# Kernel optimization log

Measured on AMD Instinct MI355X. Metric: run time of the kernel, lower is better.

## Reference

```python
import jax, jax.numpy as jnp
import numpy as np
from jax.scipy.special import logsumexp

# config (matches init_kwargs)
D_IN, D_OUT = 768, 256
P = 2
BLUR = 0.5
SCALING = 0.8
SCALING_FACTOR = 1.0
N_ITERS = 36  # fixed-length eps schedule (clamped at blur), jit-friendly


def setup_inputs() -> dict:
    key = jax.random.key(0)
    k1, k2, k3, k4 = jax.random.split(key, 4)
    d = jax.random.normal(k1, (4096, D_IN), dtype=jnp.float32)
    s1 = jax.random.normal(k2, (1024, D_IN), dtype=jnp.float32)
    s2 = jax.random.normal(k3, (1024, D_IN), dtype=jnp.float32)
    # learned projection parameter (scaled init so projected coords are O(1))
    M = jax.random.normal(k4, (D_IN, D_OUT), dtype=jnp.float32) / np.sqrt(D_IN)
    return {"d": d, "s1": s1, "s2": s2, "M": M}


def _sq_cost(u, v):
    # C[i,j] = ||u_i - v_j||^2 / 2  (geomloss p=2 cost)
    sq = (jnp.sum(u * u, -1)[:, None] + jnp.sum(v * v, -1)[None, :]
          - 2.0 * (u @ v.T))
    return jnp.maximum(sq, 0.0) * 0.5


def _softmin(eps, C, h):
    # -eps * log sum_j exp(h_j - C_ij/eps)   -> shape [C.shape[0]]
    return -eps * logsumexp(h[None, :] - C / eps, axis=1)


def _sinkhorn_divergence(x, y):
    n, m = x.shape[0], y.shape[0]
    a_log = jnp.full((n,), -np.log(n), dtype=x.dtype)  # uniform log-weights
    b_log = jnp.full((m,), -np.log(m), dtype=x.dtype)

    C_xy = _sq_cost(x, y)   # [n, m]
    C_xx = _sq_cost(x, x)   # [n, n]  (debiasing term)
    C_yy = _sq_cost(y, y)   # [m, m]

    # bounding-box diameter of the joint cloud (no grad, like geomloss)
    z = jax.lax.stop_gradient(jnp.concatenate([x, y], axis=0))
    diam = jnp.sqrt(jnp.sum((z.max(0) - z.min(0)) ** 2)) + 1e-6

    # eps-scaling schedule: scale from diameter down to blur, eps = scale^p
    scales = jnp.maximum(BLUR, diam * (SCALING ** jnp.arange(N_ITERS, dtype=x.dtype)))
    eps_list = scales ** P
    eps0 = eps_list[0]
    eps_f = jnp.asarray(BLUR ** P, dtype=x.dtype)

    # init potentials at the largest eps
    f_aa = _softmin(eps0, C_xx, a_log)
    g_bb = _softmin(eps0, C_yy, b_log)
    f_ab = _softmin(eps0, C_xy, b_log)
    g_ab = _softmin(eps0, C_xy.T, a_log)

    @jax.checkpoint
    def step(carry, eps):
        f_aa, g_bb, f_ab, g_ab = carry
        # simultaneous (Jacobi) updates, symmetrized by averaging
        ft = _softmin(eps, C_xy, b_log + g_ab / eps)
        gt = _softmin(eps, C_xy.T, a_log + f_ab / eps)
        f_aa = 0.5 * (f_aa + _softmin(eps, C_xx, a_log + f_aa / eps))
        g_bb = 0.5 * (g_bb + _softmin(eps, C_yy, b_log + g_bb / eps))
        f_ab = 0.5 * (f_ab + ft)
        g_ab = 0.5 * (g_ab + gt)
        return (f_aa, g_bb, f_ab, g_ab), None

    (f_aa, g_bb, f_ab, g_ab), _ = jax.lax.scan(
        step, (f_aa, g_bb, f_ab, g_ab), eps_list)

    # final non-averaged extrapolation at eps = blur^p
    f_ab_n = _softmin(eps_f, C_xy, b_log + g_ab / eps_f)
    g_ab_n = _softmin(eps_f, C_xy.T, a_log + f_ab / eps_f)
    f_aa_n = _softmin(eps_f, C_xx, a_log + f_aa / eps_f)
    g_bb_n = _softmin(eps_f, C_yy, b_log + g_bb / eps_f)

    # debiased divergence with uniform weights: <a, f_ab - f_aa> + <b, g_ab - g_bb>
    return jnp.mean(f_ab_n - f_aa_n) + jnp.mean(g_ab_n - g_bb_n)


def reference(d, s1, s2, M):
    xd = d @ M
    x1 = s1 @ M
    x2 = s2 @ M
    dist1 = _sinkhorn_divergence(xd, x1)
    dist2 = _sinkhorn_divergence(xd, x2)
    return jax.nn.sigmoid(SCALING_FACTOR * (dist2 - dist1))
```

## Files before the change

kernel.cpp:

```cpp
#include <hip/hip_runtime.h>
#include <hip/hip_bf16.h>
#include <math.h>

using ull = unsigned long long;
typedef unsigned short u16x8 __attribute__((ext_vector_type(8)));
typedef __attribute__((ext_vector_type(8))) short bf16x8;
typedef __attribute__((ext_vector_type(4))) float f32x4;

#define ND 4096ull
#define NS 1024ull
#define DOUT 256ull
#define DIN 768ull
#define NIT 36

constexpr ull U_CXX = 0;
constexpr ull U_CXY = U_CXX + ND*ND;
constexpr ull U_CYX = U_CXY + 2*ND*NS;
constexpr ull U_CYY = U_CYX + 2*ND*NS;
constexpr ull U_TOT = U_CYY + 2*NS*NS;
constexpr ull P_XDH = U_TOT;
constexpr ull P_XDM = P_XDH + ND*DOUT;
constexpr ull P_X1H = P_XDM + ND*DOUT;
constexpr ull P_X1M = P_X1H + NS*DOUT;
constexpr ull P_X2H = P_X1M + NS*DOUT;
constexpr ull P_X2M = P_X2H + NS*DOUT;
constexpr ull P_DH  = P_X2M + NS*DOUT;
constexpr ull P_DM  = P_DH + ND*DIN;
constexpr ull P_S1H = P_DM + ND*DIN;
constexpr ull P_S1M = P_S1H + NS*DIN;
constexpr ull P_S2H = P_S1M + NS*DIN;
constexpr ull P_S2M = P_S2H + NS*DIN;
constexpr ull P_MTH = P_S2M + NS*DIN;
constexpr ull P_MTM = P_MTH + DOUT*DIN;
constexpr ull U_END = P_MTM + DOUT*DIN;

constexpr ull O_XD   = U_END / 2;
constexpr ull O_X1   = O_XD + ND*DOUT;
constexpr ull O_X2   = O_X1 + NS*DOUT;
constexpr ull O_MT   = O_X2 + NS*DOUT;
constexpr ull O_ND_  = O_MT + DOUT*DIN;
constexpr ull O_N1   = O_ND_ + ND;
constexpr ull O_N2   = O_N1 + NS;
constexpr ull O_FAB  = O_N2 + NS;
constexpr ull O_GAB  = O_FAB + 4*ND;
constexpr ull O_FAA  = O_GAB + 4*NS;
constexpr ull O_GBB  = O_FAA + 4*ND;
constexpr ull O_FABN = O_GBB + 4*NS;
constexpr ull O_GABN = O_FABN + 2*ND;
constexpr ull O_FAAN = O_GABN + 2*NS;
constexpr ull O_GBBN = O_FAAN + 2*ND;
constexpr ull O_EPS  = O_GBBN + 2*NS;
constexpr ull O_QS   = O_EPS + 2*NIT;
constexpr ull O_DIST = O_QS + 2;
constexpr ull WS_FLOATS = O_DIST + 2;
constexpr ull O_PMIN = O_MT;
constexpr ull O_PMAX = O_MT + 96*256;

constexpr float LOG2E = 1.4426950408889634f;
constexpr float LN2   = 0.69314718055994531f;
constexpr float A_LOG2 = -12.0f;
constexpr float B_LOG2 = -10.0f;

__device__ __forceinline__ float wave_max(float v) {
    #pragma unroll
    for (int o = 32; o; o >>= 1) v = fmaxf(v, __shfl_xor(v, o));
    return v;
}
__device__ __forceinline__ float wave_sum(float v) {
    #pragma unroll
    for (int o = 32; o; o >>= 1) v += __shfl_xor(v, o);
    return v;
}

__device__ __forceinline__ unsigned short f2bf_rn(float x) {
    union { float f; unsigned u; } v; v.f = x;
    const unsigned r = v.u + 0x7FFFu + ((v.u >> 16) & 1u);
    return (unsigned short)(r >> 16);
}
__device__ __forceinline__ float bf2f(unsigned short b) {
    union { unsigned u; float f; } v; v.u = ((unsigned)b) << 16; return v.f;
}

__global__ __launch_bounds__(256)
void transpose_M_k(const float* __restrict__ M, float* __restrict__ Mt)
{
    int idx = blockIdx.x * 256 + threadIdx.x;
    int r = idx >> 8;
    int c = idx & 255;
    Mt[(size_t)c * DIN + r] = M[idx];
}

__global__ __launch_bounds__(256)
void pack_bf16_gen(const float* __restrict__ X,
                   unsigned short* __restrict__ Phi, unsigned short* __restrict__ Pmi,
                   int KB)
{
    const int p = blockIdx.x;
    const int t = threadIdx.x;
    const int K = KB * 32;
    for (int s = t; s < KB * 64; s += 256) {
        const int kb = s >> 6, l = s & 63;
        const int row = p * 16 + (l & 15);
        const int k0 = kb * 32 + ((l >> 4) << 3);
        const float* src = X + (ull)row * K + k0;
        u16x8 hi, mi;
        #pragma unroll
        for (int e = 0; e < 8; e++) {
            const float x = src[e];
            const unsigned short h = f2bf_rn(x);
            hi[e] = h;
            mi[e] = f2bf_rn(x - bf2f(h));
        }
        const ull o = (((ull)p * KB + kb) * 64 + l) * 8;
        *(u16x8*)&Phi[o] = hi;
        *(u16x8*)&Pmi[o] = mi;
    }
}

__global__ __launch_bounds__(256)
void gemm_proj_mfma(const unsigned short* __restrict__ Ahi, const unsigned short* __restrict__ Ami,
                    const unsigned short* __restrict__ Bhi, const unsigned short* __restrict__ Bmi,
                    float* __restrict__ C, int N, int KB)
{
    const int l = threadIdx.x & 63;
    const int w = threadIdx.x >> 6;
    const int n0 = blockIdx.x * 64, m0 = blockIdx.y * 128;
    const int pA0 = (m0 >> 4) + w * 2;
    const int pB0 = n0 >> 4;
    f32x4 acc[2][4] = {};
    for (int kb = 0; kb < KB; kb++) {
        const ull a0o = (((ull)(pA0 + 0) * KB + kb) * 64 + l) * 8;
        const ull a1o = (((ull)(pA0 + 1) * KB + kb) * 64 + l) * 8;
        const bf16x8 aH0 = *(const bf16x8*)&Ahi[a0o];
        const bf16x8 aM0 = *(const bf16x8*)&Ami[a0o];
        const bf16x8 aH1 = *(const bf16x8*)&Ahi[a1o];
        const bf16x8 aM1 = *(const bf16x8*)&Ami[a1o];
        #pragma unroll
        for (int j = 0; j < 4; j++) {
            const ull bo = (((ull)(pB0 + j) * KB + kb) * 64 + l) * 8;
            const bf16x8 bH = *(const bf16x8*)&Bhi[bo];
            const bf16x8 bM = *(const bf16x8*)&Bmi[bo];
            acc[0][j] = __builtin_amdgcn_mfma_f32_16x16x32_bf16(aH0, bH, acc[0][j], 0, 0, 0);
            acc[0][j] = __builtin_amdgcn_mfma_f32_16x16x32_bf16(aH0, bM, acc[0][j], 0, 0, 0);
            acc[0][j] = __builtin_amdgcn_mfma_f32_16x16x32_bf16(aM0, bH, acc[0][j], 0, 0, 0);
            acc[1][j] = __builtin_amdgcn_mfma_f32_16x16x32_bf16(aH1, bH, acc[1][j], 0, 0, 0);
            acc[1][j] = __builtin_amdgcn_mfma_f32_16x16x32_bf16(aH1, bM, acc[1][j], 0, 0, 0);
            acc[1][j] = __builtin_amdgcn_mfma_f32_16x16x32_bf16(aM1, bH, acc[1][j], 0, 0, 0);
        }
    }
    const int col = l & 15;
    #pragma unroll
    for (int i = 0; i < 2; i++) {
        const int row0 = m0 + w * 32 + i * 16 + ((l >> 4) << 2);
        #pragma unroll
        for (int r = 0; r < 4; r++) {
            const ull rowb = (ull)(row0 + r) * N + n0;
            #pragma unroll
            for (int j = 0; j < 4; j++)
                C[rowb + j * 16 + col] = acc[i][j][r];
        }
    }
}

__device__ __forceinline__ unsigned int quant16(float c, float s) {
    return __float2uint_rn(fminf(c * s, 65535.0f));
}

__global__ __launch_bounds__(256)
void gemm_cost_mfma(const unsigned short* __restrict__ Ahi, const unsigned short* __restrict__ Ami,
                    const unsigned short* __restrict__ Bhi, const unsigned short* __restrict__ Bmi,
                    unsigned short* __restrict__ C,
                    const float* __restrict__ na, const float* __restrict__ nb,
                    const float* __restrict__ qsp, int N)
{
    const int l = threadIdx.x & 63;
    const int w = threadIdx.x >> 6;
    const int n0 = blockIdx.x * 64, m0 = blockIdx.y * 128;
    const int pA0 = (m0 >> 4) + w * 2;
    const int pB0 = n0 >> 4;
    f32x4 acc[2][4] = {};
    #pragma unroll
    for (int kb = 0; kb < 8; kb++) {
        const ull a0o = (((ull)(pA0 + 0) * 8 + kb) * 64 + l) * 8;
        const ull a1o = (((ull)(pA0 + 1) * 8 + kb) * 64 + l) * 8;
        const bf16x8 aH0 = *(const bf16x8*)&Ahi[a0o];
        const bf16x8 aM0 = *(const bf16x8*)&Ami[a0o];
        const bf16x8 aH1 = *(const bf16x8*)&Ahi[a1o];
        const bf16x8 aM1 = *(const bf16x8*)&Ami[a1o];
        #pragma unroll
        for (int j = 0; j < 4; j++) {
            const ull bo = (((ull)(pB0 + j) * 8 + kb) * 64 + l) * 8;
            const bf16x8 bH = *(const bf16x8*)&Bhi[bo];
            const bf16x8 bM = *(const bf16x8*)&Bmi[bo];
            acc[0][j] = __builtin_amdgcn_mfma_f32_16x16x32_bf16(aH0, bH, acc[0][j], 0, 0, 0);
            acc[0][j] = __builtin_amdgcn_mfma_f32_16x16x32_bf16(aH0, bM, acc[0][j], 0, 0, 0);
            acc[0][j] = __builtin_amdgcn_mfma_f32_16x16x32_bf16(aM0, bH, acc[0][j], 0, 0, 0);
            acc[1][j] = __builtin_amdgcn_mfma_f32_16x16x32_bf16(aH1, bH, acc[1][j], 0, 0, 0);
            acc[1][j] = __builtin_amdgcn_mfma_f32_16x16x32_bf16(aH1, bM, acc[1][j], 0, 0, 0);
            acc[1][j] = __builtin_amdgcn_mfma_f32_16x16x32_bf16(aM1, bH, acc[1][j], 0, 0, 0);
        }
    }
    const float s = qsp[0];
    const int col = l & 15;
    float nbj[4];
    #pragma unroll
    for (int j = 0; j < 4; j++) nbj[j] = nb[n0 + j * 16 + col];
    #pragma unroll
    for (int i = 0; i < 2; i++) {
        const int row0 = m0 + w * 32 + i * 16 + ((l >> 4) << 2);
        #pragma unroll
        for (int r = 0; r < 4; r++) {
            const float nar = na[row0 + r];
            const ull rowb = (ull)(row0 + r) * N + n0;
            #pragma unroll
            for (int j = 0; j < 4; j++)
                C[rowb + j * 16 + col] =
                    (unsigned short)quant16(0.5f * fmaxf(nar + nbj[j] - 2.0f * acc[i][j][r], 0.0f), s);
        }
    }
}

__global__ __launch_bounds__(256)
void row_norm(const float* __restrict__ x, float* __restrict__ o)
{
    const int i = blockIdx.x;
    const float v = x[(size_t)i * DOUT + threadIdx.x];
    float s = wave_sum(v * v);
    __shared__ float red[4];
    const int wid = threadIdx.x >> 6, lane = threadIdx.x & 63;
    if (lane == 0) red[wid] = s;
    __syncthreads();
    if (threadIdx.x == 0) o[i] = red[0] + red[1] + red[2] + red[3];
}

__global__ __launch_bounds__(256)
void colminmax_k(const float* __restrict__ xd, const float* __restrict__ x1,
                 const float* __restrict__ x2, float* __restrict__ ws)
{
    const int b = blockIdx.x, c = threadIdx.x;
    const float* src; int r0;
    if (b < 64)      { src = xd; r0 = b * 64; }
    else if (b < 80) { src = x1; r0 = (b - 64) * 64; }
    else             { src = x2; r0 = (b - 80) * 64; }
    float mn = 3.4e38f, mx = -3.4e38f;
    for (int r = 0; r < 64; r++) {
        const float v = src[(size_t)(r0 + r) * DOUT + c];
        mn = fminf(mn, v); mx = fmaxf(mx, v);
    }
    ws[O_PMIN + (ull)b * 256 + c] = mn;
    ws[O_PMAX + (ull)b * 256 + c] = mx;
}

__global__ __launch_bounds__(256)
void eps_k(float* __restrict__ ws)
{
    const int c = threadIdx.x;
    const float* pmin = ws + O_PMIN;
    const float* pmax = ws + O_PMAX;
    float mnd = 3.4e38f, mxd = -3.4e38f;
    float mn1 = 3.4e38f, mx1 = -3.4e38f;
    float mn2 = 3.4e38f, mx2 = -3.4e38f;
    for (int b = 0;  b < 64; b++) { mnd = fminf(mnd, pmin[b*256+c]); mxd = fmaxf(mxd, pmax[b*256+c]); }
    for (int b = 64; b < 80; b++) { mn1 = fminf(mn1, pmin[b*256+c]); mx1 = fmaxf(mx1, pmax[b*256+c]); }
    for (int b = 80; b < 96; b++) { mn2 = fminf(mn2, pmin[b*256+c]); mx2 = fmaxf(mx2, pmax[b*256+c]); }
    const float d1 = fmaxf(mxd, mx1) - fminf(mnd, mn1);
    const float d2 = fmaxf(mxd, mx2) - fminf(mnd, mn2);
    float s1 = wave_sum(d1 * d1);
    float s2 = wave_sum(d2 * d2);
    __shared__ float r1[4], r2[4];
    const int wid = c >> 6, lane = c & 63;
    if (lane == 0) { r1[wid] = s1; r2[wid] = s2; }
    __syncthreads();
    if (c == 0) {
        const float d1s = r1[0]+r1[1]+r1[2]+r1[3];
        const float d2s = r2[0]+r2[1]+r2[2]+r2[3];
        const float cb = 0.5f * fmaxf(d1s, d2s) * 1.02f + 1.0f;
        ws[O_QS]     = 65535.0f / cb;
        ws[O_QS + 1] = cb / 65535.0f;
    }
    if (c < 2 * NIT) {
        const int div = c / NIT, tt = c % NIT;
        const float ss = div ? (r2[0]+r2[1]+r2[2]+r2[3]) : (r1[0]+r1[1]+r1[2]+r1[3]);
        const float diam = sqrtf(ss) + 1e-6f;
        const float sc = fmaxf(0.5f, diam * powf(0.8f, (float)tt));
        ws[O_EPS + (ull)div * NIT + tt] = sc * sc;
    }
}

__device__ __forceinline__ void softmin_1k(
    const unsigned short* __restrict__ Cseg, const float* __restrict__ hseg,
    float hc2, float ie2, float qsc, int lane, float& mO, float& sO)
{
    float v[16];
    #pragma unroll
    for (int c = 0; c < 2; c++) {
        const int off = c * 512 + lane * 8;
        const u16x8 q = *(const u16x8*)&Cseg[off];
        if (hseg) {
            const float4 ha = *(const float4*)&hseg[off];
            const float4 hb = *(const float4*)&hseg[off + 4];
            const float hv[8] = {ha.x, ha.y, ha.z, ha.w, hb.x, hb.y, hb.z, hb.w};
            #pragma unroll
            for (int e = 0; e < 8; e++)
                v[c*8 + e] = fmaf((float)q[e], qsc, fmaf(hv[e], ie2, hc2));
        } else {
            #pragma unroll
            for (int e = 0; e < 8; e++)
                v[c*8 + e] = fmaf((float)q[e], qsc, hc2);
        }
    }
    float m = v[0];
    #pragma unroll
    for (int k = 1; k < 16; k++) m = fmaxf(m, v[k]);
    m = wave_max(m);
    float s = 0.0f;
    #pragma unroll
    for (int k = 0; k < 16; k++) s += exp2f(v[k] - m);
    sO = wave_sum(s);
    mO = m;
}

__global__ __launch_bounds__(256)
void sinkhorn_phase(float* __restrict__ ws, int phase, int t)
{
    __shared__ float mS[8], sS[8];
    const unsigned short* uq = (const unsigned short*)ws;
    const int wid = threadIdx.x >> 6, lane = threadIdx.x & 63;
    const float qs = ws[O_QS + 1];
    int rb, wb;
    if (phase == 0) { rb = 0; wb = 0; }
    else { rb = t & 1; wb = rb ^ 1; }
    const int b = blockIdx.x;

    if (b < 2048) {
        const int div = b >> 10;
        const int i = ((b & 1023) << 2) + wid;
        const float eps = (phase == 2) ? 0.25f : ws[O_EPS + (ull)div * NIT + t];
        const float ie2 = LOG2E / eps, qsc = -qs * ie2;
        const unsigned short* Crow = uq + U_CXY + (ull)div * ND * NS + (ull)i * NS;
        const float* h    = phase ? (ws + O_GAB + ((ull)div * 2 + rb) * NS) : nullptr;
        const float* self = ws + O_FAB + ((ull)div * 2 + rb) * ND;
        float* outp = (phase == 2) ? (ws + O_FABN + (ull)div * ND)
                                   : (ws + O_FAB + ((ull)div * 2 + wb) * ND);
        float m, s;
        softmin_1k(Crow, h, B_LOG2, ie2, qsc, lane, m, s);
        if (lane == 0) {
            float res = -eps * LN2 * (m + log2f(s));
            if (phase == 1) res = 0.5f * (self[i] + res);
            outp[i] = res;
        }
    } else if (b < 4096) {
        const int q = b - 2048, div = q >> 10, j = q & 1023;
        const float eps = (phase == 2) ? 0.25f : ws[O_EPS + (ull)div * NIT + t];
        const float ie2 = LOG2E / eps, qsc = -qs * ie2;
        const unsigned short* Cseg = uq + U_CYX + (ull)div * ND * NS + (ull)j * ND + wid * 1024;
        const float* h    = phase ? (ws + O_FAB + ((ull)div * 2 + rb) * ND + wid * 1024) : nullptr;
        const float* self = ws + O_GAB + ((ull)div * 2 + rb) * NS;
        float* outp = (phase == 2) ? (ws + O_GABN + (ull)div * NS)
                                   : (ws + O_GAB + ((ull)div * 2 + wb) * NS);
        float m, s;
        softmin_1k(Cseg, h, A_LOG2, ie2, qsc, lane, m, s);
        if (lane == 0) { mS[wid] = m; sS[wid] = s; }
        __syncthreads();
        if (threadIdx.x == 0) {
            const float m0 = fmaxf(fmaxf(mS[0], mS[1]), fmaxf(mS[2], mS[3]));
            const float st = sS[0]*exp2f(mS[0]-m0) + sS[1]*exp2f(mS[1]-m0)
                           + sS[2]*exp2f(mS[2]-m0) + sS[3]*exp2f(mS[3]-m0);
            float res = -eps * LN2 * (m0 + log2f(st));
            if (phase == 1) res = 0.5f * (self[j] + res);
            outp[j] = res;
        }
    } else if (b < 8192) {
        const int i = b - 4096;
        const float eps0 = (phase == 2) ? 0.25f : ws[O_EPS + t];
        const float eps1 = (phase == 2) ? 0.25f : ws[O_EPS + NIT + t];
        const float ie0 = LOG2E / eps0, qs0 = -qs * ie0;
        const float ie1 = LOG2E / eps1, qs1 = -qs * ie1;
        const unsigned short* Cseg = uq + U_CXX + (ull)i * ND + wid * 1024;
        const float* h0b = ws + O_FAA + (ull)rb * ND;
        const float* h1b = ws + O_FAA + (2ull + rb) * ND;
        float* out0 = (phase == 2) ? (ws + O_FAAN)      : (ws + O_FAA + (ull)wb * ND);
        float* out1 = (phase == 2) ? (ws + O_FAAN + ND) : (ws + O_FAA + (2ull + wb) * ND);
        float v0[16], v1[16];
        #pragma unroll
        for (int c = 0; c < 2; c++) {
            const int off = c * 512 + lane * 8;
            const u16x8 q = *(const u16x8*)&Cseg[off];
            float cq[8];
            #pragma unroll
            for (int e = 0; e < 8; e++) cq[e] = (float)q[e];
            if (phase) {
                const int go = wid * 1024 + off;
                const float4 a0 = *(const float4*)&h0b[go];
                const float4 b0 = *(const float4*)&h0b[go + 4];
                const float4 a1 = *(const float4*)&h1b[go];
                const float4 b1 = *(const float4*)&h1b[go + 4];
                const float h0v[8] = {a0.x, a0.y, a0.z, a0.w, b0.x, b0.y, b0.z, b0.w};
                const float h1v[8] = {a1.x, a1.y, a1.z, a1.w, b1.x, b1.y, b1.z, b1.w};
                #pragma unroll
                for (int e = 0; e < 8; e++) {
                    v0[c*8 + e] = fmaf(cq[e], qs0, fmaf(h0v[e], ie0, A_LOG2));
                    v1[c*8 + e] = fmaf(cq[e], qs1, fmaf(h1v[e], ie1, A_LOG2));
                }
            } else {
                #pragma unroll
                for (int e = 0; e < 8; e++) {
                    v0[c*8 + e] = fmaf(cq[e], qs0, A_LOG2);
                    v1[c*8 + e] = fmaf(cq[e], qs1, A_LOG2);
                }
            }
        }
        float m0 = v0[0], m1 = v1[0];
        #pragma unroll
        for (int k = 1; k < 16; k++) { m0 = fmaxf(m0, v0[k]); m1 = fmaxf(m1, v1[k]); }
        m0 = wave_max(m0); m1 = wave_max(m1);
        float s0 = 0.0f, s1 = 0.0f;
        #pragma unroll
        for (int k = 0; k < 16; k++) { s0 += exp2f(v0[k] - m0); s1 += exp2f(v1[k] - m1); }
        s0 = wave_sum(s0); s1 = wave_sum(s1);
        if (lane == 0) { mS[wid] = m0; sS[wid] = s0; mS[4 + wid] = m1; sS[4 + wid] = s1; }
        __syncthreads();
        if (threadIdx.x == 0) {
            const float ma = fmaxf(fmaxf(mS[0], mS[1]), fmaxf(mS[2], mS[3]));
            const float sa = sS[0]*exp2f(mS[0]-ma) + sS[1]*exp2f(mS[1]-ma)
                           + sS[2]*exp2f(mS[2]-ma) + sS[3]*exp2f(mS[3]-ma);
            float r0 = -eps0 * LN2 * (ma + log2f(sa));
            if (phase == 1) r0 = 0.5f * (h0b[i] + r0);
            out0[i] = r0;
            const float mb = fmaxf(fmaxf(mS[4], mS[5]), fmaxf(mS[6], mS[7]));
            const float sb = sS[4]*exp2f(mS[4]-mb) + sS[5]*exp2f(mS[5]-mb)
                           + sS[6]*exp2f(mS[6]-mb) + sS[7]*exp2f(mS[7]-mb);
            float r1 = -eps1 * LN2 * (mb + log2f(sb));
            if (phase == 1) r1 = 0.5f * (h1b[i] + r1);
            out1[i] = r1;
        }
    } else {
        const int q = b - 8192, div = q >> 8;
        const int i = ((q & 255) << 2) + wid;
        const float eps = (phase == 2) ? 0.25f : ws[O_EPS + (ull)div * NIT + t];
        const float ie2 = LOG2E / eps, qsc = -qs * ie2;
        const unsigned short* Crow = uq + U_CYY + (ull)div * NS * NS + (ull)i * NS;
        const float* hb = ws + O_GBB + ((ull)div * 2 + rb) * NS;
        float* outp = (phase == 2) ? (ws + O_GBBN + (ull)div * NS)
                                   : (ws + O_GBB + ((ull)div * 2 + wb) * NS);
        float m, s;
        softmin_1k(Crow, phase ? hb : nullptr, B_LOG2, ie2, qsc, lane, m, s);
        if (lane == 0) {
            float res = -eps * LN2 * (m + log2f(s));
            if (phase == 1) res = 0.5f * (hb[i] + res);
            outp[i] = res;
        }
    }
}

__global__ __launch_bounds__(256)
void reduce_dist(float* __restrict__ ws)
{
    const int d = blockIdx.x;
    const int tix = threadIdx.x;
    float s = 0.0f;
    #pragma unroll
    for (int k = 0; k < 16; k++) {
        const int i = tix + k * 256;
        s += (ws[O_FABN + (ull)d * ND + i] - ws[O_FAAN + (ull)d * ND + i]) * (1.0f / 4096.0f);
    }
    #pragma unroll
    for (int k = 0; k < 4; k++) {
        const int j = tix + k * 256;
        s += (ws[O_GABN + (ull)d * NS + j] - ws[O_GBBN + (ull)d * NS + j]) * (1.0f / 1024.0f);
    }
    s = wave_sum(s);
    __shared__ float red[4];
    const int wid = tix >> 6, lane = tix & 63;
    if (lane == 0) red[wid] = s;
    __syncthreads();
    if (tix == 0) ws[O_DIST + d] = red[0] + red[1] + red[2] + red[3];
}

__global__ void finalize_k(const float* __restrict__ ws, float* __restrict__ out)
{
    const float x = ws[O_DIST + 1] - ws[O_DIST + 0];
    out[0] = 1.0f / (1.0f + expf(-x));
}

extern "C" void kernel_launch(void* const* d_in, const int* in_sizes, int n_in,
                              void* d_out, int out_size, void* d_ws, size_t ws_size,
                              hipStream_t stream)
{
    if (ws_size < WS_FLOATS * sizeof(float)) return;

    const float* dmat = (const float*)d_in[0];
    const float* s1   = (const float*)d_in[1];
    const float* s2   = (const float*)d_in[2];
    const float* M    = (const float*)d_in[3];
    float* ws  = (float*)d_ws;
    float* out = (float*)d_out;
    unsigned short* uq = (unsigned short*)d_ws;

    float* Mt = ws + O_MT;
    float* xd = ws + O_XD;
    float* x1 = ws + O_X1;
    float* x2 = ws + O_X2;

    transpose_M_k<<<768, 256, 0, stream>>>(M, Mt);
    pack_bf16_gen<<<256, 256, 0, stream>>>(dmat, uq + P_DH,  uq + P_DM,  24);
    pack_bf16_gen<<<64,  256, 0, stream>>>(s1,   uq + P_S1H, uq + P_S1M, 24);
    pack_bf16_gen<<<64,  256, 0, stream>>>(s2,   uq + P_S2H, uq + P_S2M, 24);
    pack_bf16_gen<<<16,  256, 0, stream>>>(Mt,   uq + P_MTH, uq + P_MTM, 24);
    gemm_proj_mfma<<<dim3(4, 32), 256, 0, stream>>>(uq+P_DH,  uq+P_DM,  uq+P_MTH, uq+P_MTM, xd, 256, 24);
    gemm_proj_mfma<<<dim3(4, 8),  256, 0, stream>>>(uq+P_S1H, uq+P_S1M, uq+P_MTH, uq+P_MTM, x1, 256, 24);
    gemm_proj_mfma<<<dim3(4, 8),  256, 0, stream>>>(uq+P_S2H, uq+P_S2M, uq+P_MTH, uq+P_MTM, x2, 256, 24);
    row_norm<<<4096, 256, 0, stream>>>(xd, ws + O_ND_);
    row_norm<<<1024, 256, 0, stream>>>(x1, ws + O_N1);
    row_norm<<<1024, 256, 0, stream>>>(x2, ws + O_N2);
    colminmax_k<<<96, 256, 0, stream>>>(xd, x1, x2, ws);
    eps_k<<<1, 256, 0, stream>>>(ws);
    pack_bf16_gen<<<256, 256, 0, stream>>>(xd, uq + P_XDH, uq + P_XDM, 8);
    pack_bf16_gen<<<64,  256, 0, stream>>>(x1, uq + P_X1H, uq + P_X1M, 8);
    pack_bf16_gen<<<64,  256, 0, stream>>>(x2, uq + P_X2H, uq + P_X2M, 8);
    const float* qsp = ws + O_QS;
    const float* nd_ = ws + O_ND_;
    const float* n1  = ws + O_N1;
    const float* n2  = ws + O_N2;
    gemm_cost_mfma<<<dim3(64, 32), 256, 0, stream>>>(uq+P_XDH, uq+P_XDM, uq+P_XDH, uq+P_XDM, uq + U_CXX,         nd_, nd_, qsp, 4096);
    gemm_cost_mfma<<<dim3(16, 32), 256, 0, stream>>>(uq+P_XDH, uq+P_XDM, uq+P_X1H, uq+P_X1M, uq + U_CXY,         nd_, n1,  qsp, 1024);
    gemm_cost_mfma<<<dim3(64, 8),  256, 0, stream>>>(uq+P_X1H, uq+P_X1M, uq+P_XDH, uq+P_XDM, uq + U_CYX,         n1,  nd_, qsp, 4096);
    gemm_cost_mfma<<<dim3(16, 32), 256, 0, stream>>>(uq+P_XDH, uq+P_XDM, uq+P_X2H, uq+P_X2M, uq + U_CXY + ND*NS, nd_, n2,  qsp, 1024);
    gemm_cost_mfma<<<dim3(64, 8),  256, 0, stream>>>(uq+P_X2H, uq+P_X2M, uq+P_XDH, uq+P_XDM, uq + U_CYX + ND*NS, n2,  nd_, qsp, 4096);
    gemm_cost_mfma<<<dim3(16, 8),  256, 0, stream>>>(uq+P_X1H, uq+P_X1M, uq+P_X1H, uq+P_X1M, uq + U_CYY,         n1,  n1,  qsp, 1024);
    gemm_cost_mfma<<<dim3(16, 8),  256, 0, stream>>>(uq+P_X2H, uq+P_X2M, uq+P_X2H, uq+P_X2M, uq + U_CYY + NS*NS, n2,  n2,  qsp, 1024);
    sinkhorn_phase<<<8704, 256, 0, stream>>>(ws, 0, 0);
    for (int t = 0; t < NIT; t++)
        sinkhorn_phase<<<8704, 256, 0, stream>>>(ws, 1, t);
    sinkhorn_phase<<<8704, 256, 0, stream>>>(ws, 2, 36);
    reduce_dist<<<2, 256, 0, stream>>>(ws);
    finalize_k<<<1, 1, 0, stream>>>(ws, out);
}
```

Before: 1.194 ms.

## Split softmin rows across twice as many waves with 512-thread blocks

Blocks in the Sinkhorn phase kernel go from 256 to 512 threads. Each wave now handles a 512-element segment instead of 1024, and partial max/sum pairs are merged through shared memory (pairs for the row-wise cases, eight-way for the column and self-cost cases). This doubles the wave count per iteration and halves per-thread work and register use, aiming for more memory-level parallelism on the streaming softmin. In exchange it adds block-wide syncs and extra shared-memory combine work in every block.

Result: slower. 1.376 ms (+15.2%).

```diff
diff --git a/kernel.cpp b/kernel.cpp
--- a/kernel.cpp
+++ b/kernel.cpp
@@ -287,43 +287,39 @@
     }
 }
 
-__device__ __forceinline__ void softmin_1k(
+__device__ __forceinline__ void softmin_512(
     const unsigned short* __restrict__ Cseg, const float* __restrict__ hseg,
     float hc2, float ie2, float qsc, int lane, float& mO, float& sO)
 {
-    float v[16];
-    #pragma unroll
-    for (int c = 0; c < 2; c++) {
-        const int off = c * 512 + lane * 8;
-        const u16x8 q = *(const u16x8*)&Cseg[off];
-        if (hseg) {
-            const float4 ha = *(const float4*)&hseg[off];
-            const float4 hb = *(const float4*)&hseg[off + 4];
-            const float hv[8] = {ha.x, ha.y, ha.z, ha.w, hb.x, hb.y, hb.z, hb.w};
-            #pragma unroll
-            for (int e = 0; e < 8; e++)
-                v[c*8 + e] = fmaf((float)q[e], qsc, fmaf(hv[e], ie2, hc2));
-        } else {
-            #pragma unroll
-            for (int e = 0; e < 8; e++)
-                v[c*8 + e] = fmaf((float)q[e], qsc, hc2);
-        }
+    float v[8];
+    const u16x8 q = *(const u16x8*)&Cseg[lane * 8];
+    if (hseg) {
+        const float4 ha = *(const float4*)&hseg[lane * 8];
+        const float4 hb = *(const float4*)&hseg[lane * 8 + 4];
+        const float hv[8] = {ha.x, ha.y, ha.z, ha.w, hb.x, hb.y, hb.z, hb.w};
+        #pragma unroll
+        for (int e = 0; e < 8; e++)
+            v[e] = fmaf((float)q[e], qsc, fmaf(hv[e], ie2, hc2));
+    } else {
+        #pragma unroll
+        for (int e = 0; e < 8; e++)
+            v[e] = fmaf((float)q[e], qsc, hc2);
     }
     float m = v[0];
     #pragma unroll
-    for (int k = 1; k < 16; k++) m = fmaxf(m, v[k]);
+    for (int k = 1; k < 8; k++) m = fmaxf(m, v[k]);
     m = wave_max(m);
     float s = 0.0f;
     #pragma unroll
-    for (int k = 0; k < 16; k++) s += exp2f(v[k] - m);
+    for (int k = 0; k < 8; k++) s += exp2f(v[k] - m);
     sO = wave_sum(s);
     mO = m;
 }
 
-__global__ __launch_bounds__(256)
+__global__ __launch_bounds__(512)
 void sinkhorn_phase(float* __restrict__ ws, int phase, int t)
 {
-    __shared__ float mS[8], sS[8];
+    __shared__ float mS[16], sS[16];
     const unsigned short* uq = (const unsigned short*)ws;
     const int wid = threadIdx.x >> 6, lane = threadIdx.x & 63;
     const float qs = ws[O_QS + 1];
@@ -333,19 +329,23 @@
     const int b = blockIdx.x;
 
     if (b < 2048) {
-        const int div = b >> 10;
-        const int i = ((b & 1023) << 2) + wid;
+        const int g = (b << 2) + (wid >> 1);
+        const int div = g >> 12, i = g & 4095, seg = wid & 1;
         const float eps = (phase == 2) ? 0.25f : ws[O_EPS + (ull)div * NIT + t];
         const float ie2 = LOG2E / eps, qsc = -qs * ie2;
-        const unsigned short* Crow = uq + U_CXY + (ull)div * ND * NS + (ull)i * NS;
-        const float* h    = phase ? (ws + O_GAB + ((ull)div * 2 + rb) * NS) : nullptr;
+        const unsigned short* Cseg = uq + U_CXY + (ull)div * ND * NS + (ull)i * NS + seg * 512;
+        const float* h    = phase ? (ws + O_GAB + ((ull)div * 2 + rb) * NS + seg * 512) : nullptr;
         const float* self = ws + O_FAB + ((ull)div * 2 + rb) * ND;
         float* outp = (phase == 2) ? (ws + O_FABN + (ull)div * ND)
                                    : (ws + O_FAB + ((ull)div * 2 + wb) * ND);
         float m, s;
-        softmin_1k(Crow, h, B_LOG2, ie2, qsc, lane, m, s);
-        if (lane == 0) {
-            float res = -eps * LN2 * (m + log2f(s));
+        softmin_512(Cseg, h, B_LOG2, ie2, qsc, lane, m, s);
+        if (lane == 0) { mS[wid] = m; sS[wid] = s; }
+        __syncthreads();
+        if (seg == 0 && lane == 0) {
+            const float m0 = fmaxf(mS[wid], mS[wid + 1]);
+            const float st = sS[wid]*exp2f(mS[wid]-m0) + sS[wid+1]*exp2f(mS[wid+1]-m0);
+            float res = -eps * LN2 * (m0 + log2f(st));
             if (phase == 1) res = 0.5f * (self[i] + res);
             outp[i] = res;
         }
@@ -353,19 +353,22 @@
         const int q = b - 2048, div = q >> 10, j = q & 1023;
         const float eps = (phase == 2) ? 0.25f : ws[O_EPS + (ull)div * NIT + t];
         const float ie2 = LOG2E / eps, qsc = -qs * ie2;
-        const unsigned short* Cseg = uq + U_CYX + (ull)div * ND * NS + (ull)j * ND + wid * 1024;
-        const float* h    = phase ? (ws + O_FAB + ((ull)div * 2 + rb) * ND + wid * 1024) : nullptr;
+        const unsigned short* Cseg = uq + U_CYX + (ull)div * ND * NS + (ull)j * ND + wid * 512;
+        const float* h    = phase ? (ws + O_FAB + ((ull)div * 2 + rb) * ND + wid * 512) : nullptr;
         const float* self = ws + O_GAB + ((ull)div * 2 + rb) * NS;
         float* outp = (phase == 2) ? (ws + O_GABN + (ull)div * NS)
                                    : (ws + O_GAB + ((ull)div * 2 + wb) * NS);
         float m, s;
-        softmin_1k(Cseg, h, A_LOG2, ie2, qsc, lane, m, s);
+        softmin_512(Cseg, h, A_LOG2, ie2, qsc, lane, m, s);
         if (lane == 0) { mS[wid] = m; sS[wid] = s; }
         __syncthreads();
         if (threadIdx.x == 0) {
-            const float m0 = fmaxf(fmaxf(mS[0], mS[1]), fmaxf(mS[2], mS[3]));
-            const float st = sS[0]*exp2f(mS[0]-m0) + sS[1]*exp2f(mS[1]-m0)
-                           + sS[2]*exp2f(mS[2]-m0) + sS[3]*exp2f(mS[3]-m0);
+            float m0 = mS[0];
+            #pragma unroll
+            for (int k = 1; k < 8; k++) m0 = fmaxf(m0, mS[k]);
+            float st = 0.0f;
+            #pragma unroll
+            for (int k = 0; k < 8; k++) st += sS[k] * exp2f(mS[k] - m0);
             float res = -eps * LN2 * (m0 + log2f(st));
             if (phase == 1) res = 0.5f * (self[j] + res);
             outp[j] = res;
@@ -376,21 +379,19 @@
         const float eps1 = (phase == 2) ? 0.25f : ws[O_EPS + NIT + t];
         const float ie0 = LOG2E / eps0, qs0 = -qs * ie0;
         const float ie1 = LOG2E / eps1, qs1 = -qs * ie1;
-        const unsigned short* Cseg = uq + U_CXX + (ull)i * ND + wid * 1024;
+        const unsigned short* Cseg = uq + U_CXX + (ull)i * ND + wid * 512;
         const float* h0b = ws + O_FAA + (ull)rb * ND;
         const float* h1b = ws + O_FAA + (2ull + rb) * ND;
         float* out0 = (phase == 2) ? (ws + O_FAAN)      : (ws + O_FAA + (ull)wb * ND);
         float* out1 = (phase == 2) ? (ws + O_FAAN + ND) : (ws + O_FAA + (2ull + wb) * ND);
-        float v0[16], v1[16];
-        #pragma unroll
-        for (int c = 0; c < 2; c++) {
-            const int off = c * 512 + lane * 8;
-            const u16x8 q = *(const u16x8*)&Cseg[off];
+        float v0[8], v1[8];
+        {
+            const u16x8 q = *(const u16x8*)&Cseg[lane * 8];
             float cq[8];
             #pragma unroll
             for (int e = 0; e < 8; e++) cq[e] = (float)q[e];
             if (phase) {
-                const int go = wid * 1024 + off;
+                const int go = wid * 512 + lane * 8;
                 const float4 a0 = *(const float4*)&h0b[go];
                 const float4 b0 = *(const float4*)&h0b[go + 4];
                 const float4 a1 = *(const float4*)&h1b[go];
@@ -399,54 +400,66 @@
                 const float h1v[8] = {a1.x, a1.y, a1.z, a1.w, b1.x, b1.y, b1.z, b1.w};
                 #pragma unroll
                 for (int e = 0; e < 8; e++) {
-                    v0[c*8 + e] = fmaf(cq[e], qs0, fmaf(h0v[e], ie0, A_LOG2));
-                    v1[c*8 + e] = fmaf(cq[e], qs1, fmaf(h1v[e], ie1, A_LOG2));
+                    v0[e] = fmaf(cq[e], qs0, fmaf(h0v[e], ie0, A_LOG2));
+                    v1[e] = fmaf(cq[e], qs1, fmaf(h1v[e], ie1, A_LOG2));
                 }
             } else {
                 #pragma unroll
                 for (int e = 0; e < 8; e++) {
-                    v0[c*8 + e] = fmaf(cq[e], qs0, A_LOG2);
-                    v1[c*8 + e] = fmaf(cq[e], qs1, A_LOG2);
+                    v0[e] = fmaf(cq[e], qs0, A_LOG2);
+                    v1[e] = fmaf(cq[e], qs1, A_LOG2);
                 }
             }
         }
         float m0 = v0[0], m1 = v1[0];
         #pragma unroll
-        for (int k = 1; k < 16; k++) { m0 = fmaxf(m0, v0[k]); m1 = fmaxf(m1, v1[k]); }
+        for (int k = 1; k < 8; k++) { m0 = fmaxf(m0, v0[k]); m1 = fmaxf(m1, v1[k]); }
         m0 = wave_max(m0); m1 = wave_max(m1);
         float s0 = 0.0f, s1 = 0.0f;
         #pragma unroll
-        for (int k = 0; k < 16; k++) { s0 += exp2f(v0[k] - m0); s1 += exp2f(v1[k] - m1); }
+        for (int k = 0; k < 8; k++) { s0 += exp2f(v0[k] - m0); s1 += exp2f(v1[k] - m1); }
         s0 = wave_sum(s0); s1 = wave_sum(s1);
-        if (lane == 0) { mS[wid] = m0; sS[wid] = s0; mS[4 + wid] = m1; sS[4 + wid] = s1; }
+        if (lane == 0) { mS[wid] = m0; sS[wid] = s0; mS[8 + wid] = m1; sS[8 + wid] = s1; }
         __syncthreads();
         if (threadIdx.x == 0) {
-            const float ma = fmaxf(fmaxf(mS[0], mS[1]), fmaxf(mS[2], mS[3]));
-            const float sa = sS[0]*exp2f(mS[0]-ma) + sS[1]*exp2f(mS[1]-ma)
-                           + sS[2]*exp2f(mS[2]-ma) + sS[3]*exp2f(mS[3]-ma);
+            float ma = mS[0];
+            #pragma unroll
+            for (int k = 1; k < 8; k++) ma = fmaxf(ma, mS[k]);
+            float sa = 0.0f;
+            #pragma unroll
+            for (int k = 0; k < 8; k++) sa += sS[k] * exp2f(mS[k] - ma);
             float r0 = -eps0 * LN2 * (ma + log2f(sa));
             if (phase == 1) r0 = 0.5f * (h0b[i] + r0);
             out0[i] = r0;
-            const float mb = fmaxf(fmaxf(mS[4], mS[5]), fmaxf(mS[6], mS[7]));
-            const float sb = sS[4]*exp2f(mS[4]-mb) + sS[5]*exp2f(mS[5]-mb)
-                           + sS[6]*exp2f(mS[6]-mb) + sS[7]*exp2f(mS[7]-mb);
+            float mb = mS[8];
+            #pragma unroll
+            for (int k = 9; k < 16; k++) mb = fmaxf(mb, mS[k]);
+            float sb = 0.0f;
+            #pragma unroll
+            for (int k = 8; k < 16; k++) sb += sS[k] * exp2f(mS[k] - mb);
             float r1 = -eps1 * LN2 * (mb + log2f(sb));
             if (phase == 1) r1 = 0.5f * (h1b[i] + r1);
             out1[i] = r1;
         }
     } else {
-        const int q = b - 8192, div = q >> 8;
-        const int i = ((q & 255) << 2) + wid;
+        const int q = b - 8192;
+        const int g = (q << 2) + (wid >> 1);
+        const int div = g >> 10, i = g & 1023, seg = wid & 1;
         const float eps = (phase == 2) ? 0.25f : ws[O_EPS + (ull)div * NIT + t];
         const float ie2 = LOG2E / eps, qsc = -qs * ie2;
-        const unsigned short* Crow = uq + U_CYY + (ull)div * NS * NS + (ull)i * NS;
+        const unsigned short* Cseg = uq + U_CYY + (ull)div * NS * NS + (ull)i * NS + seg * 512;
         const float* hb = ws + O_GBB + ((ull)div * 2 + rb) * NS;
+        const float* h = phase ? (hb + seg * 512) : nullptr;
         float* outp = (phase == 2) ? (ws + O_GBBN + (ull)div * NS)
                                    : (ws + O_GBB + ((ull)div * 2 + wb) * NS);
         float m, s;
-        softmin_1k(Crow, phase ? hb : nullptr, B_LOG2, ie2, qsc, lane, m, s);
-        if (lane == 0) {
-            float res = -eps * LN2 * (m + log2f(s));
+        softmin_512(Cseg, h, B_LOG2, ie2, qsc, lane, m, s);
+        if (lane == 0) { mS[wid] = m; sS[wid] = s; }
+        __syncthreads();
+        if (seg == 0 && lane == 0) {
+            const float m0 = fmaxf(mS[wid], mS[wid + 1]);
+            const float st = sS[wid]*exp2f(mS[wid]-m0) + sS[wid+1]*exp2f(mS[wid+1]-m0);
+            float res = -eps * LN2 * (m0 + log2f(st));
             if (phase == 1) res = 0.5f * (hb[i] + res);
             outp[i] = res;
         }
@@ -529,10 +542,10 @@
     gemm_cost_mfma<<<dim3(64, 8),  256, 0, stream>>>(uq+P_X2H, uq+P_X2M, uq+P_XDH, uq+P_XDM, uq + U_CYX + ND*NS, n2,  nd_, qsp, 4096);
     gemm_cost_mfma<<<dim3(16, 8),  256, 0, stream>>>(uq+P_X1H, uq+P_X1M, uq+P_X1H, uq+P_X1M, uq + U_CYY,         n1,  n1,  qsp, 1024);
     gemm_cost_mfma<<<dim3(16, 8),  256, 0, stream>>>(uq+P_X2H, uq+P_X2M, uq+P_X2H, uq+P_X2M, uq + U_CYY + NS*NS, n2,  n2,  qsp, 1024);
-    sinkhorn_phase<<<8704, 256, 0, stream>>>(ws, 0, 0);
+    sinkhorn_phase<<<8704, 512, 0, stream>>>(ws, 0, 0);
     for (int t = 0; t < NIT; t++)
-        sinkhorn_phase<<<8704, 256, 0, stream>>>(ws, 1, t);
-    sinkhorn_phase<<<8704, 256, 0, stream>>>(ws, 2, 36);
+        sinkhorn_phase<<<8704, 512, 0, stream>>>(ws, 1, t);
+    sinkhorn_phase<<<8704, 512, 0, stream>>>(ws, 2, 36);
     reduce_dist<<<2, 256, 0, stream>>>(ws);
     finalize_k<<<1, 1, 0, stream>>>(ws, out);
 }
```
